# Kernel tuning notes

Hardware: AMD Instinct MI355X
Metric: run time of the kernel (lower is better)

The kernel has to match this reference:

```python
import jax, jax.numpy as jnp
import numpy as np

N, E = 10000, 100000   # nodes, edges
C = 64                 # sphere_channels
L2 = 9                 # (lmax+1)^2 with lmax=2
H, DH, DV = 8, 16, 16  # heads, alpha channels/head, value channels/head
EC = 64                # edge scalar channels
NRBF = 128             # radial basis size
ZMAX = 90              # max_num_elements


def setup_inputs() -> dict:
    key = jax.random.key(0)
    ks = jax.random.split(key, 12)
    inp = {}
    inp["node_embedding"] = jax.random.normal(ks[0], (N, L2, C), jnp.float32)
    inp["atomic_numbers"] = jax.random.randint(ks[1], (N,), 0, ZMAX)
    inp["edge_distance"] = jax.random.uniform(ks[2], (E,), jnp.float32)
    inp["edge_index"] = jax.random.randint(ks[3], (2, E), 0, N)
    # per-edge Wigner rotation into the edge-aligned SO(2) frame
    inp["wigner"] = jax.random.normal(ks[4], (E, L2, L2), jnp.float32) / np.sqrt(L2)
    # learned parameters
    inp["atom_emb"] = jax.random.normal(ks[5], (ZMAX, EC), jnp.float32) * 0.1
    inp["W_rbf"] = jax.random.normal(ks[6], (NRBF, EC), jnp.float32) / np.sqrt(NRBF)
    inp["W_gate"] = jax.random.normal(ks[7], (EC, H * DH), jnp.float32) / np.sqrt(EC)
    inp["W_msg"] = jax.random.normal(ks[8], (2 * C, H * DH), jnp.float32) / np.sqrt(2 * C)
    inp["alpha_vec"] = jax.random.normal(ks[9], (H, DH), jnp.float32) / np.sqrt(DH)
    inp["W_val"] = jax.random.normal(ks[10], (H * DH, H * DV), jnp.float32) / np.sqrt(H * DH)
    inp["W_out"] = jax.random.normal(ks[11], (H * DV, 1), jnp.float32) / np.sqrt(H * DV)
    return inp


def reference(node_embedding, atomic_numbers, edge_distance, edge_index, wigner,
              atom_emb, W_rbf, W_gate, W_msg, alpha_vec, W_val, W_out):
    src, dst = edge_index[0], edge_index[1]
    # --- edge scalar embedding: gaussian RBF of distance + endpoint atom embeddings ---
    centers = jnp.linspace(0.0, 1.0, NRBF, dtype=node_embedding.dtype)
    width = 1.0 / NRBF
    rbf = jnp.exp(-((edge_distance[:, None] - centers) ** 2) / (2.0 * width * width))  # [E, NRBF]
    edge_scalar = jax.nn.silu(rbf @ W_rbf + atom_emb[atomic_numbers[src]] + atom_emb[atomic_numbers[dst]])  # [E, EC]
    gate = jax.nn.silu(edge_scalar @ W_gate)  # [E, H*DH]
    # --- gather endpoint embeddings and rotate into edge frame (SO3 rotation) ---
    x_s = jnp.einsum('eij,ejc->eic', wigner, node_embedding[src])  # [E, L2, C]
    x_t = jnp.einsum('eij,ejc->eic', wigner, node_embedding[dst])  # [E, L2, C]
    msg = jnp.concatenate([x_s, x_t], axis=-1) @ W_msg            # [E, L2, H*DH]
    msg = msg * gate[:, None, :]
    # --- attention logits from the invariant (l=0) component ---
    a = msg[:, 0, :].reshape(E, H, DH)
    logits = jnp.einsum('ehd,hd->eh', jax.nn.leaky_relu(a, 0.2), alpha_vec)  # [E, H]
    # --- softmax over incoming edges of each destination node ---
    m = jax.ops.segment_max(logits, dst, num_segments=N)  # [N, H]
    ex = jnp.exp(logits - m[dst])
    den = jax.ops.segment_sum(ex, dst, num_segments=N)
    attn = ex / (den[dst] + 1e-9)  # [E, H]
    # --- attention-weighted values, rotate back, scatter-sum to nodes ---
    v = (msg @ W_val).reshape(E, L2, H, DV)
    v = v * attn[:, None, :, None]
    v = jnp.einsum('eji,ejhv->eihv', wigner, v).reshape(E, L2, H * DV)  # rotate back (R^T)
    node_out = jax.ops.segment_sum(v, dst, num_segments=N)  # [N, L2, H*DV]
    out = node_out @ W_out                                   # [N, L2, 1]
    forces = out[:, 1:4, 0]                                  # narrow(1,1,3).view(-1,3)
    return forces
```

## Files before the change

### kernel.cpp

```cpp
#include <hip/hip_runtime.h>
#include <hip/hip_bf16.h>

#define NN 10000
#define NE 100000

typedef __attribute__((ext_vector_type(8))) short short8v;
typedef __attribute__((ext_vector_type(4))) float float4v;

__device__ __forceinline__ float bcast(float v, int k) {
  return __int_as_float(__builtin_amdgcn_readlane(__float_as_int(v), k));
}
__device__ __forceinline__ unsigned int enc_f(float f) {
  unsigned int u = __float_as_uint(f);
  return (u & 0x80000000u) ? ~u : (u | 0x80000000u);
}
__device__ __forceinline__ float dec_f(unsigned int u) {
  return __uint_as_float((u & 0x80000000u) ? (u & 0x7fffffffu) : ~u);
}
__device__ __forceinline__ float silu_f(float x) {
  return x / (1.0f + __expf(-x));
}
__device__ __forceinline__ void f32_hilo(float x, short& h, short& l) {
  __hip_bfloat16 bh = __float2bfloat16(x);
  float r = x - __bfloat162float(bh);
  __hip_bfloat16 bl = __float2bfloat16(r);
  h = __builtin_bit_cast(short, bh);
  l = __builtin_bit_cast(short, bl);
}
#define MFMA16(a, b, c) __builtin_amdgcn_mfma_f32_16x16x32_bf16(a, b, c, 0, 0, 0)

__global__ void prep_kernel(const float* __restrict__ W_msg, const float* __restrict__ W_val,
                            const float* __restrict__ W_out, const float* __restrict__ W_rbf,
                            const float* __restrict__ W_gate,
                            float* __restrict__ Q,
                            short* __restrict__ Wp1h, short* __restrict__ Wp1l,
                            short* __restrict__ Wp2h, short* __restrict__ Wp2l,
                            short* __restrict__ Wp3h, short* __restrict__ Wp3l,
                            short* __restrict__ Wp4h, short* __restrict__ Wp4l) {
  int i = blockIdx.x * blockDim.x + threadIdx.x;
  if (i < 1024) {
    int c = i >> 3, h = i & 7;
    float s = 0.0f;
#pragma unroll
    for (int dv = 0; dv < 16; ++dv)
      s += W_val[c * 128 + h * 16 + dv] * W_out[h * 16 + dv];
    Q[c * 8 + h] = s;
  }
  const float* W; short* ph; short* pl; int KF, Nw, local; bool tr = false;
  if (i < 8192)       { W = W_rbf;  ph = Wp1h; pl = Wp1l; KF = 4; Nw = 64;  local = i; }
  else if (i < 16384) { W = W_gate; ph = Wp2h; pl = Wp2l; KF = 2; Nw = 128; local = i - 8192; }
  else if (i < 32768) { W = W_msg;  ph = Wp3h; pl = Wp3l; KF = 4; Nw = 128; local = i - 16384; }
  else                { W = W_msg;  ph = Wp4h; pl = Wp4l; KF = 4; Nw = 128; local = i - 32768; tr = true; }
  int tile = local >> 9;
  int ln = (local >> 3) & 63;
  int j = local & 7;
  int nt = tile / KF, kf = tile % KF;
  int k = kf * 32 + 8 * (ln >> 4) + j;
  int n = nt * 16 + (ln & 15);
  float w = tr ? W[n * 128 + k] : W[k * Nw + n];
  short h, lo;
  f32_hilo(w, h, lo);
  ph[local] = h;
  pl[local] = lo;
}

__global__ __launch_bounds__(256) void pass1_kernel(
    const float* __restrict__ nb, const int* __restrict__ zn,
    const float* __restrict__ dist, const int* __restrict__ ei,
    const float* __restrict__ wig, const float* __restrict__ aemb,
    const float* __restrict__ alpha,
    const short* __restrict__ Wp1h, const short* __restrict__ Wp1l,
    const short* __restrict__ Wp2h, const short* __restrict__ Wp2l,
    const short* __restrict__ Wp3h, const short* __restrict__ Wp3l,
    float* __restrict__ logits, unsigned int* __restrict__ m_enc,
    __hip_bfloat16* __restrict__ gate_ws) {
  __shared__ __attribute__((aligned(16))) float es_s[4][16][68];
  __shared__ __attribute__((aligned(16))) float xc_s[4][16][132];
  const int tid = threadIdx.x;
  const int lane = tid & 63;
  const int wid = tid >> 6;
  const int g = lane >> 4;
  const int col = lane & 15;
  const int e0 = (blockIdx.x * 4 + wid) * 16;

#pragma unroll 4
  for (int e = 0; e < 16; ++e) {
    int eu = e0 + e; if (eu >= NE) eu = NE - 1;
    int se = __builtin_amdgcn_readfirstlane(ei[eu]);
    int de = __builtin_amdgcn_readfirstlane(ei[NE + eu]);
    const float* __restrict__ pw = wig + (size_t)eu * 81;
    const float* __restrict__ ps = nb + (size_t)se * 576 + lane;
    const float* __restrict__ pt = nb + (size_t)de * 576 + lane;
    float xs = 0.0f, xt = 0.0f;
#pragma unroll
    for (int j = 0; j < 9; ++j) {
      float wj = pw[j];
      xs += wj * ps[j * 64];
      xt += wj * pt[j * 64];
    }
    xc_s[wid][e][lane] = xs;
    xc_s[wid][e][64 + lane] = xt;
  }

  int ecol = e0 + col; if (ecol >= NE) ecol = NE - 1;
  const float d = dist[ecol];
  short8v a1h[4], a1l[4];
#pragma unroll
  for (int kf = 0; kf < 4; ++kf) {
#pragma unroll
    for (int j = 0; j < 8; ++j) {
      int k = kf * 32 + 8 * g + j;
      float t = d - (float)k * (1.0f / 127.0f);
      float v = __expf(-8192.0f * t * t);
      short h, lo; f32_hilo(v, h, lo);
      a1h[kf][j] = h; a1l[kf][j] = lo;
    }
  }

  const float4v z4 = {0.0f, 0.0f, 0.0f, 0.0f};

  float4v acc1[4];
#pragma unroll
  for (int nt = 0; nt < 4; ++nt) {
    float4v a = z4;
#pragma unroll
    for (int kf = 0; kf < 4; ++kf) {
      short8v bh = *(const short8v*)(Wp1h + ((nt * 4 + kf) * 64 + lane) * 8);
      short8v bl = *(const short8v*)(Wp1l + ((nt * 4 + kf) * 64 + lane) * 8);
      a = MFMA16(a1h[kf], bh, a);
      a = MFMA16(a1h[kf], bl, a);
      a = MFMA16(a1l[kf], bh, a);
    }
    acc1[nt] = a;
  }

  int dn_r[4];
#pragma unroll
  for (int r = 0; r < 4; ++r) {
    int er = e0 + 4 * g + r;
    int erc = er < NE ? er : NE - 1;
    int sn = ei[erc];
    dn_r[r] = ei[NE + erc];
    int zs = zn[sn], zd = zn[dn_r[r]];
#pragma unroll
    for (int nt = 0; nt < 4; ++nt) {
      float b = aemb[zs * 64 + nt * 16 + col] + aemb[zd * 64 + nt * 16 + col];
      es_s[wid][4 * g + r][nt * 16 + col] = silu_f(acc1[nt][r] + b);
    }
  }
  __syncthreads();

  short8v a2h[2], a2l[2];
#pragma unroll
  for (int kf = 0; kf < 2; ++kf) {
    const float* p = &es_s[wid][col][kf * 32 + 8 * g];
    float4v v0 = *(const float4v*)p;
    float4v v1 = *(const float4v*)(p + 4);
#pragma unroll
    for (int j = 0; j < 4; ++j) {
      short h, lo;
      f32_hilo(v0[j], h, lo); a2h[kf][j] = h;     a2l[kf][j] = lo;
      f32_hilo(v1[j], h, lo); a2h[kf][4 + j] = h; a2l[kf][4 + j] = lo;
    }
  }

  float gate_r[8][4];
#pragma unroll
  for (int nt = 0; nt < 8; ++nt) {
    float4v a = z4;
#pragma unroll
    for (int kf = 0; kf < 2; ++kf) {
      short8v bh = *(const short8v*)(Wp2h + ((nt * 2 + kf) * 64 + lane) * 8);
      short8v bl = *(const short8v*)(Wp2l + ((nt * 2 + kf) * 64 + lane) * 8);
      a = MFMA16(a2h[kf], bh, a);
      a = MFMA16(a2h[kf], bl, a);
      a = MFMA16(a2l[kf], bh, a);
    }
#pragma unroll
    for (int r = 0; r < 4; ++r) {
      float gv = silu_f(a[r]);
      gate_r[nt][r] = gv;
      int er = e0 + 4 * g + r;
      if (er < NE)
        gate_ws[(size_t)er * 128 + nt * 16 + col] = __float2bfloat16(gv);
    }
  }

  short8v a3h[4], a3l[4];
#pragma unroll
  for (int kf = 0; kf < 4; ++kf) {
    const float* p = &xc_s[wid][col][kf * 32 + 8 * g];
    float4v v0 = *(const float4v*)p;
    float4v v1 = *(const float4v*)(p + 4);
#pragma unroll
    for (int j = 0; j < 4; ++j) {
      short h, lo;
      f32_hilo(v0[j], h, lo); a3h[kf][j] = h;     a3l[kf][j] = lo;
      f32_hilo(v1[j], h, lo); a3h[kf][4 + j] = h; a3l[kf][4 + j] = lo;
    }
  }

#pragma unroll
  for (int nt = 0; nt < 8; ++nt) {
    float4v a = z4;
#pragma unroll
    for (int kf = 0; kf < 4; ++kf) {
      short8v bh = *(const short8v*)(Wp3h + ((nt * 4 + kf) * 64 + lane) * 8);
      short8v bl = *(const short8v*)(Wp3l + ((nt * 4 + kf) * 64 + lane) * 8);
      a = MFMA16(a3h[kf], bh, a);
      a = MFMA16(a3h[kf], bl, a);
      a = MFMA16(a3l[kf], bh, a);
    }
    float al = alpha[nt * 16 + col];
#pragma unroll
    for (int r = 0; r < 4; ++r) {
      float v = a[r] * gate_r[nt][r];
      v = v > 0.0f ? v : 0.2f * v;
      v *= al;
#pragma unroll
      for (int off = 1; off < 16; off <<= 1) v += __shfl_xor(v, off);
      int er = e0 + 4 * g + r;
      if (col == 0 && er < NE) {
        logits[(size_t)er * 8 + nt] = v;
        atomicMax(&m_enc[dn_r[r] * 8 + nt], enc_f(v));
      }
    }
  }
}

__global__ void pass2_kernel(const float* __restrict__ logits,
                             const int* __restrict__ ei,
                             const unsigned int* __restrict__ m_enc,
                             float* __restrict__ den) {
  int i = blockIdx.x * blockDim.x + threadIdx.x;
  if (i >= NE * 8) return;
  int e = i >> 3, h = i & 7;
  int dn = ei[NE + e];
  float mm = dec_f(m_enc[dn * 8 + h]);
  atomicAdd(&den[dn * 8 + h], __expf(logits[i] - mm));
}

__global__ __launch_bounds__(256) void pass3_kernel(
    const float* __restrict__ nb, const int* __restrict__ ei,
    const float* __restrict__ wig, const float* __restrict__ logits,
    const unsigned int* __restrict__ m_enc, const float* __restrict__ den,
    const __hip_bfloat16* __restrict__ gate_ws, const float* __restrict__ Q,
    const short* __restrict__ Wp4h, const short* __restrict__ Wp4l,
    float* __restrict__ out) {
  __shared__ __attribute__((aligned(16))) float attn_s[4][16][8];
  __shared__ __attribute__((aligned(16))) float x_s[4][16][132];
  const int tid = threadIdx.x;
  const int lane = tid & 63;
  const int wid = tid >> 6;
  const int g = lane >> 4;
  const int col = lane & 15;
  const int e0 = (blockIdx.x * 4 + wid) * 16;

#pragma unroll
  for (int half = 0; half < 2; ++half) {
    int i = half * 64 + lane;
    int e = i >> 3, h = i & 7;
    int ec = e0 + e; if (ec >= NE) ec = NE - 1;
    int dn = ei[NE + ec];
    float l = logits[(size_t)ec * 8 + h];
    float mm = dec_f(m_enc[dn * 8 + h]);
    float dv = den[dn * 8 + h];
    attn_s[wid][e][h] = __expf(l - mm) / (dv + 1e-9f);
  }

  float q0[8], q1[8];
#pragma unroll
  for (int h = 0; h < 8; ++h) {
    q0[h] = Q[lane * 8 + h];
    q1[h] = Q[(lane + 64) * 8 + h];
  }
#pragma unroll 4
  for (int e = 0; e < 16; ++e) {
    int ec = e0 + e; if (ec >= NE) ec = NE - 1;
    float4v a0 = *(const float4v*)&attn_s[wid][e][0];
    float4v a1 = *(const float4v*)&attn_s[wid][e][4];
    float wv0 = 0.0f, wv1 = 0.0f;
#pragma unroll
    for (int h = 0; h < 4; ++h) {
      wv0 += q0[h] * a0[h] + q0[4 + h] * a1[h];
      wv1 += q1[h] * a0[h] + q1[4 + h] * a1[h];
    }
    float gg0 = __bfloat162float(gate_ws[(size_t)ec * 128 + lane]);
    float gg1 = __bfloat162float(gate_ws[(size_t)ec * 128 + 64 + lane]);
    x_s[wid][e][lane] = gg0 * wv0;
    x_s[wid][e][64 + lane] = gg1 * wv1;
  }

  short8v ah[4], al[4];
#pragma unroll
  for (int kf = 0; kf < 4; ++kf) {
    const float* p = &x_s[wid][col][kf * 32 + 8 * g];
    float4v v0 = *(const float4v*)p;
    float4v v1 = *(const float4v*)(p + 4);
#pragma unroll
    for (int j = 0; j < 4; ++j) {
      short h, lo;
      f32_hilo(v0[j], h, lo); ah[kf][j] = h;     al[kf][j] = lo;
      f32_hilo(v1[j], h, lo); ah[kf][4 + j] = h; al[kf][4 + j] = lo;
    }
  }
  const float4v z4 = {0.0f, 0.0f, 0.0f, 0.0f};
  float4v acc[8];
#pragma unroll
  for (int nt = 0; nt < 8; ++nt) {
    float4v a = z4;
#pragma unroll
    for (int kf = 0; kf < 4; ++kf) {
      short8v bh = *(const short8v*)(Wp4h + ((nt * 4 + kf) * 64 + lane) * 8);
      short8v bl = *(const short8v*)(Wp4l + ((nt * 4 + kf) * 64 + lane) * 8);
      a = MFMA16(ah[kf], bh, a);
      a = MFMA16(ah[kf], bl, a);
      a = MFMA16(al[kf], bh, a);
    }
    acc[nt] = a;
  }
#pragma unroll
  for (int nt = 0; nt < 8; ++nt)
#pragma unroll
    for (int r = 0; r < 4; ++r)
      x_s[wid][4 * g + r][nt * 16 + col] = acc[nt][r];

  const int cg = col * 4;
#pragma unroll
  for (int it = 0; it < 4; ++it) {
    int e = it * 4 + g;
    int eu = e0 + e;
    bool valid = eu < NE;
    int ec = valid ? eu : NE - 1;
    int se = ei[ec], de = ei[NE + ec];
    float4v t0 = *(const float4v*)&x_s[wid][e][cg];
    float4v t1 = *(const float4v*)&x_s[wid][e][64 + cg];
    const float* ps = nb + (size_t)se * 576 + cg;
    const float* pt = nb + (size_t)de * 576 + cg;
    float dj[9];
#pragma unroll
    for (int j = 0; j < 9; ++j) {
      float4v a = *(const float4v*)(ps + j * 64);
      float4v b = *(const float4v*)(pt + j * 64);
      dj[j] = a[0] * t0[0] + a[1] * t0[1] + a[2] * t0[2] + a[3] * t0[3] +
              b[0] * t1[0] + b[1] * t1[1] + b[2] * t1[2] + b[3] * t1[3];
    }
#pragma unroll
    for (int j = 0; j < 9; ++j)
#pragma unroll
      for (int off = 1; off < 16; off <<= 1) dj[j] += __shfl_xor(dj[j], off);

    const float* we = wig + (size_t)ec * 81;
    int ls = col < 9 ? col : 8;
    float s_l = 0.0f;
#pragma unroll
    for (int jp = 0; jp < 9; ++jp) s_l += we[ls * 9 + jp] * dj[jp];
    int lc = (col >= 1 && col <= 3) ? col : 1;
    float f = 0.0f;
#pragma unroll
    for (int j = 0; j < 9; ++j)
      f += __shfl(s_l, (lane & 48) + j) * we[j * 9 + lc];
    if (col >= 1 && col <= 3 && valid)
      atomicAdd(&out[de * 3 + (col - 1)], f);
  }
}

extern "C" void kernel_launch(void* const* d_in, const int* in_sizes, int n_in,
                              void* d_out, int out_size, void* d_ws, size_t ws_size,
                              hipStream_t stream) {
  const float* nb = (const float*)d_in[0];
  const int* zn = (const int*)d_in[1];
  const float* dist = (const float*)d_in[2];
  const int* ei = (const int*)d_in[3];
  const float* wig = (const float*)d_in[4];
  const float* aemb = (const float*)d_in[5];
  const float* W_rbf = (const float*)d_in[6];
  const float* W_gate = (const float*)d_in[7];
  const float* W_msg = (const float*)d_in[8];
  const float* alpha = (const float*)d_in[9];
  const float* W_val = (const float*)d_in[10];
  const float* W_out = (const float*)d_in[11];
  float* out = (float*)d_out;

  char* p = (char*)d_ws;
  float* Q = (float*)p;                   p += 1024 * 4;
  unsigned int* m_enc = (unsigned int*)p; p += (size_t)NN * 8 * 4;
  float* den = (float*)p;                 p += (size_t)NN * 8 * 4;
  float* logits = (float*)p;              p += (size_t)NE * 8 * 4;
  __hip_bfloat16* gate_ws = (__hip_bfloat16*)p; p += (size_t)NE * 128 * 2;
  short* Wp1h = (short*)p; p += 8192 * 2;
  short* Wp1l = (short*)p; p += 8192 * 2;
  short* Wp2h = (short*)p; p += 8192 * 2;
  short* Wp2l = (short*)p; p += 8192 * 2;
  short* Wp3h = (short*)p; p += 16384 * 2;
  short* Wp3l = (short*)p; p += 16384 * 2;
  short* Wp4h = (short*)p; p += 16384 * 2;
  short* Wp4l = (short*)p; p += 16384 * 2;

  hipMemsetAsync(d_out, 0, (size_t)NN * 3 * 4, stream);
  hipMemsetAsync(m_enc, 0, (size_t)NN * 8 * 4, stream);
  hipMemsetAsync(den, 0, (size_t)NN * 8 * 4, stream);

  prep_kernel<<<192, 256, 0, stream>>>(W_msg, W_val, W_out, W_rbf, W_gate, Q,
                                       Wp1h, Wp1l, Wp2h, Wp2l, Wp3h, Wp3l, Wp4h, Wp4l);
  pass1_kernel<<<(NE + 63) / 64, 256, 0, stream>>>(nb, zn, dist, ei, wig, aemb, alpha,
                                                   Wp1h, Wp1l, Wp2h, Wp2l, Wp3h, Wp3l,
                                                   logits, m_enc, gate_ws);
  pass2_kernel<<<(NE * 8 + 255) / 256, 256, 0, stream>>>(logits, ei, m_enc, den);
  pass3_kernel<<<(NE + 63) / 64, 256, 0, stream>>>(nb, ei, wig, logits, m_enc, den,
                                                   gate_ws, Q, Wp4h, Wp4l, out);
}
```

Baseline: 325.2 us.

## Software-pipeline edge gathers and prefetch edge indices in pass1 and pass3

In pass1, all edge indices for a wave are loaded at once and broadcast with readlane. The per-edge node and Wigner gathers are double-buffered in registers so the loads for the next edges are in flight while the current rotation is computed. The two shared buffers are merged into one per-wave buffer, which lets the block-wide __syncthreads go. Both kernels get a launch-bounds occupancy hint, and pass3 prefetches its src/dst indices, loads the bf16 gate values as packed pairs, and batches the node-embedding loads ahead of the dot products. The extra in-flight registers raise register pressure, which could limit occupancy or cause spills.

```diff
diff --git a/kernel.cpp b/kernel.cpp
--- a/kernel.cpp
+++ b/kernel.cpp
@@ -9,6 +9,9 @@
 
 __device__ __forceinline__ float bcast(float v, int k) {
   return __int_as_float(__builtin_amdgcn_readlane(__float_as_int(v), k));
+}
+__device__ __forceinline__ int bcast_i(int v, int k) {
+  return __builtin_amdgcn_readlane(v, k);
 }
 __device__ __forceinline__ unsigned int enc_f(float f) {
   unsigned int u = __float_as_uint(f);
@@ -28,6 +31,24 @@
   l = __builtin_bit_cast(short, bl);
 }
 #define MFMA16(a, b, c) __builtin_amdgcn_mfma_f32_16x16x32_bf16(a, b, c, 0, 0, 0)
+
+__device__ __forceinline__ void g_issue(const float* __restrict__ nb,
+                                        const float* __restrict__ wig,
+                                        int idx_v, int e0, int e, int lane,
+                                        float (&VS)[9], float (&VT)[9], float (&WJ)[9]) {
+  int se_ = bcast_i(idx_v, e);
+  int de_ = bcast_i(idx_v, 16 + e);
+  int ec_ = (e0 + e < NE) ? e0 + e : NE - 1;
+  const float* __restrict__ ps_ = nb + (size_t)se_ * 576 + lane;
+  const float* __restrict__ pt_ = nb + (size_t)de_ * 576 + lane;
+  const float* __restrict__ pw_ = wig + (size_t)ec_ * 81;
+#pragma unroll
+  for (int j = 0; j < 9; ++j) {
+    VS[j] = ps_[j * 64];
+    VT[j] = pt_[j * 64];
+    WJ[j] = pw_[j];
+  }
+}
 
 __global__ void prep_kernel(const float* __restrict__ W_msg, const float* __restrict__ W_val,
                             const float* __restrict__ W_out, const float* __restrict__ W_rbf,
@@ -64,7 +85,7 @@
   pl[local] = lo;
 }
 
-__global__ __launch_bounds__(256) void pass1_kernel(
+__global__ __launch_bounds__(256, 3) void pass1_kernel(
     const float* __restrict__ nb, const int* __restrict__ zn,
     const float* __restrict__ dist, const int* __restrict__ ei,
     const float* __restrict__ wig, const float* __restrict__ aemb,
@@ -74,8 +95,7 @@
     const short* __restrict__ Wp3h, const short* __restrict__ Wp3l,
     float* __restrict__ logits, unsigned int* __restrict__ m_enc,
     __hip_bfloat16* __restrict__ gate_ws) {
-  __shared__ __attribute__((aligned(16))) float es_s[4][16][68];
-  __shared__ __attribute__((aligned(16))) float xc_s[4][16][132];
+  __shared__ __attribute__((aligned(16))) float xe_s[4][16][132];
   const int tid = threadIdx.x;
   const int lane = tid & 63;
   const int wid = tid >> 6;
@@ -83,27 +103,37 @@
   const int col = lane & 15;
   const int e0 = (blockIdx.x * 4 + wid) * 16;
 
-#pragma unroll 4
-  for (int e = 0; e < 16; ++e) {
-    int eu = e0 + e; if (eu >= NE) eu = NE - 1;
-    int se = __builtin_amdgcn_readfirstlane(ei[eu]);
-    int de = __builtin_amdgcn_readfirstlane(ei[NE + eu]);
-    const float* __restrict__ pw = wig + (size_t)eu * 81;
-    const float* __restrict__ ps = nb + (size_t)se * 576 + lane;
-    const float* __restrict__ pt = nb + (size_t)de * 576 + lane;
-    float xs = 0.0f, xt = 0.0f;
-#pragma unroll
-    for (int j = 0; j < 9; ++j) {
-      float wj = pw[j];
-      xs += wj * ps[j * 64];
-      xt += wj * pt[j * 64];
-    }
-    xc_s[wid][e][lane] = xs;
-    xc_s[wid][e][64 + lane] = xt;
-  }
+  int l16 = lane & 15;
+  int ecl16 = (e0 + l16 < NE) ? e0 + l16 : NE - 1;
+  int idx_v = 0;
+  if (lane < 32) idx_v = ei[(lane < 16 ? 0 : NE) + ecl16];
 
   int ecol = e0 + col; if (ecol >= NE) ecol = NE - 1;
   const float d = dist[ecol];
+
+  float vs0[9], vt0[9], wj0[9], vs1[9], vt1[9], wj1[9];
+  g_issue(nb, wig, idx_v, e0, 0, lane, vs0, vt0, wj0);
+  g_issue(nb, wig, idx_v, e0, 1, lane, vs1, vt1, wj1);
+#pragma unroll
+  for (int e = 0; e < 16; e += 2) {
+    {
+      float xs = 0.0f, xt = 0.0f;
+#pragma unroll
+      for (int j = 0; j < 9; ++j) { xs += wj0[j] * vs0[j]; xt += wj0[j] * vt0[j]; }
+      xe_s[wid][e][lane] = xs;
+      xe_s[wid][e][64 + lane] = xt;
+    }
+    if (e + 2 < 16) g_issue(nb, wig, idx_v, e0, e + 2, lane, vs0, vt0, wj0);
+    {
+      float xs = 0.0f, xt = 0.0f;
+#pragma unroll
+      for (int j = 0; j < 9; ++j) { xs += wj1[j] * vs1[j]; xt += wj1[j] * vt1[j]; }
+      xe_s[wid][e + 1][lane] = xs;
+      xe_s[wid][e + 1][64 + lane] = xt;
+    }
+    if (e + 3 < 16) g_issue(nb, wig, idx_v, e0, e + 3, lane, vs1, vt1, wj1);
+  }
+
   short8v a1h[4], a1l[4];
 #pragma unroll
   for (int kf = 0; kf < 4; ++kf) {
@@ -117,6 +147,20 @@
     }
   }
 
+  short8v a3h[4], a3l[4];
+#pragma unroll
+  for (int kf = 0; kf < 4; ++kf) {
+    const float* p = &xe_s[wid][col][kf * 32 + 8 * g];
+    float4v v0 = *(const float4v*)p;
+    float4v v1 = *(const float4v*)(p + 4);
+#pragma unroll
+    for (int j = 0; j < 4; ++j) {
+      short h, lo;
+      f32_hilo(v0[j], h, lo); a3h[kf][j] = h;     a3l[kf][j] = lo;
+      f32_hilo(v1[j], h, lo); a3h[kf][4 + j] = h; a3l[kf][4 + j] = lo;
+    }
+  }
+
   const float4v z4 = {0.0f, 0.0f, 0.0f, 0.0f};
 
   float4v acc1[4];
@@ -137,23 +181,20 @@
   int dn_r[4];
 #pragma unroll
   for (int r = 0; r < 4; ++r) {
-    int er = e0 + 4 * g + r;
-    int erc = er < NE ? er : NE - 1;
-    int sn = ei[erc];
-    dn_r[r] = ei[NE + erc];
+    int sn = __shfl(idx_v, 4 * g + r);
+    dn_r[r] = __shfl(idx_v, 16 + 4 * g + r);
     int zs = zn[sn], zd = zn[dn_r[r]];
 #pragma unroll
     for (int nt = 0; nt < 4; ++nt) {
       float b = aemb[zs * 64 + nt * 16 + col] + aemb[zd * 64 + nt * 16 + col];
-      es_s[wid][4 * g + r][nt * 16 + col] = silu_f(acc1[nt][r] + b);
-    }
-  }
-  __syncthreads();
+      xe_s[wid][4 * g + r][nt * 16 + col] = silu_f(acc1[nt][r] + b);
+    }
+  }
 
   short8v a2h[2], a2l[2];
 #pragma unroll
   for (int kf = 0; kf < 2; ++kf) {
-    const float* p = &es_s[wid][col][kf * 32 + 8 * g];
+    const float* p = &xe_s[wid][col][kf * 32 + 8 * g];
     float4v v0 = *(const float4v*)p;
     float4v v1 = *(const float4v*)(p + 4);
 #pragma unroll
@@ -183,20 +224,6 @@
       int er = e0 + 4 * g + r;
       if (er < NE)
         gate_ws[(size_t)er * 128 + nt * 16 + col] = __float2bfloat16(gv);
-    }
-  }
-
-  short8v a3h[4], a3l[4];
-#pragma unroll
-  for (int kf = 0; kf < 4; ++kf) {
-    const float* p = &xc_s[wid][col][kf * 32 + 8 * g];
-    float4v v0 = *(const float4v*)p;
-    float4v v1 = *(const float4v*)(p + 4);
-#pragma unroll
-    for (int j = 0; j < 4; ++j) {
-      short h, lo;
-      f32_hilo(v0[j], h, lo); a3h[kf][j] = h;     a3l[kf][j] = lo;
-      f32_hilo(v1[j], h, lo); a3h[kf][4 + j] = h; a3l[kf][4 + j] = lo;
     }
   }
 
@@ -240,7 +267,7 @@
   atomicAdd(&den[dn * 8 + h], __expf(logits[i] - mm));
 }
 
-__global__ __launch_bounds__(256) void pass3_kernel(
+__global__ __launch_bounds__(256, 3) void pass3_kernel(
     const float* __restrict__ nb, const int* __restrict__ ei,
     const float* __restrict__ wig, const float* __restrict__ logits,
     const unsigned int* __restrict__ m_enc, const float* __restrict__ den,
@@ -256,6 +283,15 @@
   const int col = lane & 15;
   const int e0 = (blockIdx.x * 4 + wid) * 16;
 
+  int se_d[4], de_d[4];
+#pragma unroll
+  for (int it = 0; it < 4; ++it) {
+    int e = it * 4 + g;
+    int ec = (e0 + e < NE) ? e0 + e : NE - 1;
+    se_d[it] = ei[ec];
+    de_d[it] = ei[NE + ec];
+  }
+
 #pragma unroll
   for (int half = 0; half < 2; ++half) {
     int i = half * 64 + lane;
@@ -271,8 +307,8 @@
   float q0[8], q1[8];
 #pragma unroll
   for (int h = 0; h < 8; ++h) {
-    q0[h] = Q[lane * 8 + h];
-    q1[h] = Q[(lane + 64) * 8 + h];
+    q0[h] = Q[(2 * lane) * 8 + h];
+    q1[h] = Q[(2 * lane + 1) * 8 + h];
   }
 #pragma unroll 4
   for (int e = 0; e < 16; ++e) {
@@ -285,10 +321,11 @@
       wv0 += q0[h] * a0[h] + q0[4 + h] * a1[h];
       wv1 += q1[h] * a0[h] + q1[4 + h] * a1[h];
     }
-    float gg0 = __bfloat162float(gate_ws[(size_t)ec * 128 + lane]);
-    float gg1 = __bfloat162float(gate_ws[(size_t)ec * 128 + 64 + lane]);
-    x_s[wid][e][lane] = gg0 * wv0;
-    x_s[wid][e][64 + lane] = gg1 * wv1;
+    unsigned int gp = *(const unsigned int*)(gate_ws + (size_t)ec * 128 + 2 * lane);
+    float gg0 = __uint_as_float((gp & 0xffffu) << 16);
+    float gg1 = __uint_as_float((gp & 0xffff0000u));
+    float2 uu; uu.x = gg0 * wv0; uu.y = gg1 * wv1;
+    *(float2*)&x_s[wid][e][2 * lane] = uu;
   }
 
   short8v ah[4], al[4];
@@ -305,7 +342,6 @@
     }
   }
   const float4v z4 = {0.0f, 0.0f, 0.0f, 0.0f};
-  float4v acc[8];
 #pragma unroll
   for (int nt = 0; nt < 8; ++nt) {
     float4v a = z4;
@@ -317,13 +353,10 @@
       a = MFMA16(ah[kf], bl, a);
       a = MFMA16(al[kf], bh, a);
     }
-    acc[nt] = a;
-  }
-#pragma unroll
-  for (int nt = 0; nt < 8; ++nt)
 #pragma unroll
     for (int r = 0; r < 4; ++r)
-      x_s[wid][4 * g + r][nt * 16 + col] = acc[nt][r];
+      x_s[wid][4 * g + r][nt * 16 + col] = a[r];
+  }
 
   const int cg = col * 4;
 #pragma unroll
@@ -332,18 +365,21 @@
     int eu = e0 + e;
     bool valid = eu < NE;
     int ec = valid ? eu : NE - 1;
-    int se = ei[ec], de = ei[NE + ec];
     float4v t0 = *(const float4v*)&x_s[wid][e][cg];
     float4v t1 = *(const float4v*)&x_s[wid][e][64 + cg];
-    const float* ps = nb + (size_t)se * 576 + cg;
-    const float* pt = nb + (size_t)de * 576 + cg;
+    const float* ps = nb + (size_t)se_d[it] * 576 + cg;
+    const float* pt = nb + (size_t)de_d[it] * 576 + cg;
+    float4v pa[9], pb[9];
+#pragma unroll
+    for (int j = 0; j < 9; ++j) {
+      pa[j] = *(const float4v*)(ps + j * 64);
+      pb[j] = *(const float4v*)(pt + j * 64);
+    }
     float dj[9];
 #pragma unroll
     for (int j = 0; j < 9; ++j) {
-      float4v a = *(const float4v*)(ps + j * 64);
-      float4v b = *(const float4v*)(pt + j * 64);
-      dj[j] = a[0] * t0[0] + a[1] * t0[1] + a[2] * t0[2] + a[3] * t0[3] +
-              b[0] * t1[0] + b[1] * t1[1] + b[2] * t1[2] + b[3] * t1[3];
+      dj[j] = pa[j][0] * t0[0] + pa[j][1] * t0[1] + pa[j][2] * t0[2] + pa[j][3] * t0[3] +
+              pb[j][0] * t1[0] + pb[j][1] * t1[1] + pb[j][2] * t1[2] + pb[j][3] * t1[3];
     }
 #pragma unroll
     for (int j = 0; j < 9; ++j)
@@ -361,7 +397,7 @@
     for (int j = 0; j < 9; ++j)
       f += __shfl(s_l, (lane & 48) + j) * we[j * 9 + lc];
     if (col >= 1 && col <= 3 && valid)
-      atomicAdd(&out[de * 3 + (col - 1)], f);
+      atomicAdd(&out[de_d[it] * 3 + (col - 1)], f);
   }
 }
 
```

Measured after the change: 307.0 us. 1.06x faster.

## Split gather and scatter phases into separate one-edge-per-wave kernels

Applied to the files above, without the earlier changes.

The node-embedding gather plus Wigner rotation moves out of pass1 into its own kernel that handles one edge per wave and writes the rotated features to a workspace. The back-rotation and force scatter likewise move out of pass3 into a separate one-edge-per-wave kernel that reads an intermediate buffer. Separately, pass1 now fetches edge indices once and broadcasts them with shuffles, drops a block barrier and sets launch bounds for occupancy; pass3a reads packed bf16 gate pairs. The aim is more memory parallelism and fewer serial per-wave gather loops, paid for with an extra write and read of an E x 128 float workspace and two more kernel launches.

```diff
diff --git a/kernel.cpp b/kernel.cpp
--- a/kernel.cpp
+++ b/kernel.cpp
@@ -7,9 +7,6 @@
 typedef __attribute__((ext_vector_type(8))) short short8v;
 typedef __attribute__((ext_vector_type(4))) float float4v;
 
-__device__ __forceinline__ float bcast(float v, int k) {
-  return __int_as_float(__builtin_amdgcn_readlane(__float_as_int(v), k));
-}
 __device__ __forceinline__ unsigned int enc_f(float f) {
   unsigned int u = __float_as_uint(f);
   return (u & 0x80000000u) ? ~u : (u | 0x80000000u);
@@ -64,18 +61,39 @@
   pl[local] = lo;
 }
 
-__global__ __launch_bounds__(256) void pass1_kernel(
-    const float* __restrict__ nb, const int* __restrict__ zn,
-    const float* __restrict__ dist, const int* __restrict__ ei,
-    const float* __restrict__ wig, const float* __restrict__ aemb,
-    const float* __restrict__ alpha,
+__global__ __launch_bounds__(256) void gather1_kernel(
+    const float* __restrict__ nb, const int* __restrict__ ei,
+    const float* __restrict__ wig, float* __restrict__ xc) {
+  const int lane = threadIdx.x & 63;
+  const int e = blockIdx.x * 4 + (threadIdx.x >> 6);
+  int se = ei[e], de = ei[NE + e];
+  const float* __restrict__ pw = wig + (size_t)e * 81;
+  const float* __restrict__ ps = nb + (size_t)se * 576 + lane;
+  const float* __restrict__ pt = nb + (size_t)de * 576 + lane;
+  float vs[9], vt[9], wj[9];
+#pragma unroll
+  for (int j = 0; j < 9; ++j) {
+    vs[j] = ps[j * 64];
+    vt[j] = pt[j * 64];
+    wj[j] = pw[j];
+  }
+  float xs = 0.0f, xt = 0.0f;
+#pragma unroll
+  for (int j = 0; j < 9; ++j) { xs += wj[j] * vs[j]; xt += wj[j] * vt[j]; }
+  xc[(size_t)e * 128 + lane] = xs;
+  xc[(size_t)e * 128 + 64 + lane] = xt;
+}
+
+__global__ __launch_bounds__(256, 3) void pass1_kernel(
+    const int* __restrict__ zn, const float* __restrict__ dist,
+    const int* __restrict__ ei, const float* __restrict__ aemb,
+    const float* __restrict__ alpha, const float* __restrict__ xc,
     const short* __restrict__ Wp1h, const short* __restrict__ Wp1l,
     const short* __restrict__ Wp2h, const short* __restrict__ Wp2l,
     const short* __restrict__ Wp3h, const short* __restrict__ Wp3l,
     float* __restrict__ logits, unsigned int* __restrict__ m_enc,
     __hip_bfloat16* __restrict__ gate_ws) {
   __shared__ __attribute__((aligned(16))) float es_s[4][16][68];
-  __shared__ __attribute__((aligned(16))) float xc_s[4][16][132];
   const int tid = threadIdx.x;
   const int lane = tid & 63;
   const int wid = tid >> 6;
@@ -83,27 +101,22 @@
   const int col = lane & 15;
   const int e0 = (blockIdx.x * 4 + wid) * 16;
 
-#pragma unroll 4
-  for (int e = 0; e < 16; ++e) {
-    int eu = e0 + e; if (eu >= NE) eu = NE - 1;
-    int se = __builtin_amdgcn_readfirstlane(ei[eu]);
-    int de = __builtin_amdgcn_readfirstlane(ei[NE + eu]);
-    const float* __restrict__ pw = wig + (size_t)eu * 81;
-    const float* __restrict__ ps = nb + (size_t)se * 576 + lane;
-    const float* __restrict__ pt = nb + (size_t)de * 576 + lane;
-    float xs = 0.0f, xt = 0.0f;
-#pragma unroll
-    for (int j = 0; j < 9; ++j) {
-      float wj = pw[j];
-      xs += wj * ps[j * 64];
-      xt += wj * pt[j * 64];
-    }
-    xc_s[wid][e][lane] = xs;
-    xc_s[wid][e][64 + lane] = xt;
-  }
+  int l16 = lane & 15;
+  int ecl16 = (e0 + l16 < NE) ? e0 + l16 : NE - 1;
+  int idx_v = 0;
+  if (lane < 32) idx_v = ei[(lane < 16 ? 0 : NE) + ecl16];
 
   int ecol = e0 + col; if (ecol >= NE) ecol = NE - 1;
   const float d = dist[ecol];
+
+  const float* __restrict__ xr = xc + (size_t)ecol * 128;
+  float4v xv[4][2];
+#pragma unroll
+  for (int kf = 0; kf < 4; ++kf) {
+    xv[kf][0] = *(const float4v*)(xr + kf * 32 + 8 * g);
+    xv[kf][1] = *(const float4v*)(xr + kf * 32 + 8 * g + 4);
+  }
+
   short8v a1h[4], a1l[4];
 #pragma unroll
   for (int kf = 0; kf < 4; ++kf) {
@@ -137,10 +150,8 @@
   int dn_r[4];
 #pragma unroll
   for (int r = 0; r < 4; ++r) {
-    int er = e0 + 4 * g + r;
-    int erc = er < NE ? er : NE - 1;
-    int sn = ei[erc];
-    dn_r[r] = ei[NE + erc];
+    int sn = __shfl(idx_v, 4 * g + r);
+    dn_r[r] = __shfl(idx_v, 16 + 4 * g + r);
     int zs = zn[sn], zd = zn[dn_r[r]];
 #pragma unroll
     for (int nt = 0; nt < 4; ++nt) {
@@ -148,7 +159,6 @@
       es_s[wid][4 * g + r][nt * 16 + col] = silu_f(acc1[nt][r] + b);
     }
   }
-  __syncthreads();
 
   short8v a2h[2], a2l[2];
 #pragma unroll
@@ -189,14 +199,11 @@
   short8v a3h[4], a3l[4];
 #pragma unroll
   for (int kf = 0; kf < 4; ++kf) {
-    const float* p = &xc_s[wid][col][kf * 32 + 8 * g];
-    float4v v0 = *(const float4v*)p;
-    float4v v1 = *(const float4v*)(p + 4);
 #pragma unroll
     for (int j = 0; j < 4; ++j) {
       short h, lo;
-      f32_hilo(v0[j], h, lo); a3h[kf][j] = h;     a3l[kf][j] = lo;
-      f32_hilo(v1[j], h, lo); a3h[kf][4 + j] = h; a3l[kf][4 + j] = lo;
+      f32_hilo(xv[kf][0][j], h, lo); a3h[kf][j] = h;     a3l[kf][j] = lo;
+      f32_hilo(xv[kf][1][j], h, lo); a3h[kf][4 + j] = h; a3l[kf][4 + j] = lo;
     }
   }
 
@@ -240,13 +247,12 @@
   atomicAdd(&den[dn * 8 + h], __expf(logits[i] - mm));
 }
 
-__global__ __launch_bounds__(256) void pass3_kernel(
-    const float* __restrict__ nb, const int* __restrict__ ei,
-    const float* __restrict__ wig, const float* __restrict__ logits,
+__global__ __launch_bounds__(256, 3) void pass3a_kernel(
+    const int* __restrict__ ei, const float* __restrict__ logits,
     const unsigned int* __restrict__ m_enc, const float* __restrict__ den,
     const __hip_bfloat16* __restrict__ gate_ws, const float* __restrict__ Q,
     const short* __restrict__ Wp4h, const short* __restrict__ Wp4l,
-    float* __restrict__ out) {
+    float* __restrict__ t_ws) {
   __shared__ __attribute__((aligned(16))) float attn_s[4][16][8];
   __shared__ __attribute__((aligned(16))) float x_s[4][16][132];
   const int tid = threadIdx.x;
@@ -271,8 +277,8 @@
   float q0[8], q1[8];
 #pragma unroll
   for (int h = 0; h < 8; ++h) {
-    q0[h] = Q[lane * 8 + h];
-    q1[h] = Q[(lane + 64) * 8 + h];
+    q0[h] = Q[(2 * lane) * 8 + h];
+    q1[h] = Q[(2 * lane + 1) * 8 + h];
   }
 #pragma unroll 4
   for (int e = 0; e < 16; ++e) {
@@ -285,10 +291,11 @@
       wv0 += q0[h] * a0[h] + q0[4 + h] * a1[h];
       wv1 += q1[h] * a0[h] + q1[4 + h] * a1[h];
     }
-    float gg0 = __bfloat162float(gate_ws[(size_t)ec * 128 + lane]);
-    float gg1 = __bfloat162float(gate_ws[(size_t)ec * 128 + 64 + lane]);
-    x_s[wid][e][lane] = gg0 * wv0;
-    x_s[wid][e][64 + lane] = gg1 * wv1;
+    unsigned int gp = *(const unsigned int*)(gate_ws + (size_t)ec * 128 + 2 * lane);
+    float gg0 = __uint_as_float((gp & 0xffffu) << 16);
+    float gg1 = __uint_as_float((gp & 0xffff0000u));
+    float2 uu; uu.x = gg0 * wv0; uu.y = gg1 * wv1;
+    *(float2*)&x_s[wid][e][2 * lane] = uu;
   }
 
   short8v ah[4], al[4];
@@ -305,7 +312,6 @@
     }
   }
   const float4v z4 = {0.0f, 0.0f, 0.0f, 0.0f};
-  float4v acc[8];
 #pragma unroll
   for (int nt = 0; nt < 8; ++nt) {
     float4v a = z4;
@@ -317,52 +323,47 @@
       a = MFMA16(ah[kf], bl, a);
       a = MFMA16(al[kf], bh, a);
     }
-    acc[nt] = a;
-  }
-#pragma unroll
-  for (int nt = 0; nt < 8; ++nt)
-#pragma unroll
-    for (int r = 0; r < 4; ++r)
-      x_s[wid][4 * g + r][nt * 16 + col] = acc[nt][r];
-
-  const int cg = col * 4;
-#pragma unroll
-  for (int it = 0; it < 4; ++it) {
-    int e = it * 4 + g;
-    int eu = e0 + e;
-    bool valid = eu < NE;
-    int ec = valid ? eu : NE - 1;
-    int se = ei[ec], de = ei[NE + ec];
-    float4v t0 = *(const float4v*)&x_s[wid][e][cg];
-    float4v t1 = *(const float4v*)&x_s[wid][e][64 + cg];
-    const float* ps = nb + (size_t)se * 576 + cg;
-    const float* pt = nb + (size_t)de * 576 + cg;
-    float dj[9];
-#pragma unroll
-    for (int j = 0; j < 9; ++j) {
-      float4v a = *(const float4v*)(ps + j * 64);
-      float4v b = *(const float4v*)(pt + j * 64);
-      dj[j] = a[0] * t0[0] + a[1] * t0[1] + a[2] * t0[2] + a[3] * t0[3] +
-              b[0] * t1[0] + b[1] * t1[1] + b[2] * t1[2] + b[3] * t1[3];
-    }
-#pragma unroll
-    for (int j = 0; j < 9; ++j)
-#pragma unroll
-      for (int off = 1; off < 16; off <<= 1) dj[j] += __shfl_xor(dj[j], off);
-
-    const float* we = wig + (size_t)ec * 81;
-    int ls = col < 9 ? col : 8;
-    float s_l = 0.0f;
-#pragma unroll
-    for (int jp = 0; jp < 9; ++jp) s_l += we[ls * 9 + jp] * dj[jp];
-    int lc = (col >= 1 && col <= 3) ? col : 1;
-    float f = 0.0f;
-#pragma unroll
-    for (int j = 0; j < 9; ++j)
-      f += __shfl(s_l, (lane & 48) + j) * we[j * 9 + lc];
-    if (col >= 1 && col <= 3 && valid)
-      atomicAdd(&out[de * 3 + (col - 1)], f);
-  }
+#pragma unroll
+    for (int r = 0; r < 4; ++r) {
+      int er = e0 + 4 * g + r;
+      if (er < NE)
+        t_ws[(size_t)er * 128 + nt * 16 + col] = a[r];
+    }
+  }
+}
+
+__global__ __launch_bounds__(256) void pass3b_kernel(
+    const float* __restrict__ nb, const int* __restrict__ ei,
+    const float* __restrict__ wig, const float* __restrict__ t_ws,
+    float* __restrict__ out) {
+  const int lane = threadIdx.x & 63;
+  const int e = blockIdx.x * 4 + (threadIdx.x >> 6);
+  int se = ei[e], de = ei[NE + e];
+  float t0 = t_ws[(size_t)e * 128 + lane];
+  float t1 = t_ws[(size_t)e * 128 + 64 + lane];
+  const float* __restrict__ ps = nb + (size_t)se * 576 + lane;
+  const float* __restrict__ pt = nb + (size_t)de * 576 + lane;
+  float p[9];
+#pragma unroll
+  for (int j = 0; j < 9; ++j)
+    p[j] = ps[j * 64] * t0 + pt[j * 64] * t1;
+#pragma unroll
+  for (int off = 1; off < 64; off <<= 1)
+#pragma unroll
+    for (int j = 0; j < 9; ++j) p[j] += __shfl_xor(p[j], off);
+
+  const float* __restrict__ we = wig + (size_t)e * 81;
+  int ls = lane < 9 ? lane : 8;
+  float s_l = 0.0f;
+#pragma unroll
+  for (int jp = 0; jp < 9; ++jp) s_l += we[ls * 9 + jp] * p[jp];
+  int lc = (lane >= 1 && lane <= 3) ? lane : 1;
+  float f = 0.0f;
+#pragma unroll
+  for (int j = 0; j < 9; ++j)
+    f += __shfl(s_l, j) * we[j * 9 + lc];
+  if (lane >= 1 && lane <= 3)
+    atomicAdd(&out[de * 3 + (lane - 1)], f);
 }
 
 extern "C" void kernel_launch(void* const* d_in, const int* in_sizes, int n_in,
@@ -396,6 +397,8 @@
   short* Wp3l = (short*)p; p += 16384 * 2;
   short* Wp4h = (short*)p; p += 16384 * 2;
   short* Wp4l = (short*)p; p += 16384 * 2;
+  float* xc_ws = (float*)p;               p += (size_t)NE * 128 * 4;
+  float* t_ws = xc_ws;
 
   hipMemsetAsync(d_out, 0, (size_t)NN * 3 * 4, stream);
   hipMemsetAsync(m_enc, 0, (size_t)NN * 8 * 4, stream);
@@ -403,10 +406,12 @@
 
   prep_kernel<<<192, 256, 0, stream>>>(W_msg, W_val, W_out, W_rbf, W_gate, Q,
                                        Wp1h, Wp1l, Wp2h, Wp2l, Wp3h, Wp3l, Wp4h, Wp4l);
-  pass1_kernel<<<(NE + 63) / 64, 256, 0, stream>>>(nb, zn, dist, ei, wig, aemb, alpha,
+  gather1_kernel<<<NE / 4, 256, 0, stream>>>(nb, ei, wig, xc_ws);
+  pass1_kernel<<<(NE + 63) / 64, 256, 0, stream>>>(zn, dist, ei, aemb, alpha, xc_ws,
                                                    Wp1h, Wp1l, Wp2h, Wp2l, Wp3h, Wp3l,
                                                    logits, m_enc, gate_ws);
   pass2_kernel<<<(NE * 8 + 255) / 256, 256, 0, stream>>>(logits, ei, m_enc, den);
-  pass3_kernel<<<(NE + 63) / 64, 256, 0, stream>>>(nb, ei, wig, logits, m_enc, den,
-                                                   gate_ws, Q, Wp4h, Wp4l, out);
-}
+  pass3a_kernel<<<(NE + 63) / 64, 256, 0, stream>>>(ei, logits, m_enc, den,
+                                                    gate_ws, Q, Wp4h, Wp4l, t_ws);
+  pass3b_kernel<<<NE / 4, 256, 0, stream>>>(nb, ei, wig, t_ws, out);
+}
```

Result: slower. 344.6 us (+5.9%).
